# Optimization experiments

Hardware: AMD Instinct MI355X
Metric: run time of the kernel (lower is better)

Reference implementation:

```python
import jax, jax.numpy as jnp
import numpy as np

NUM_ENTS = 100000
NUM_RELS = 237
IN_CH, OUT_CH, KER = 1, 32, 9
IN_DIM = 200
K = 10
OUT_DIM = K * IN_DIM                      # 2000
L_IN = OUT_DIM // IN_CH                   # 2000
L_OUT = (L_IN - KER) // 1 + 1             # 1992
FC_LEN = OUT_CH * L_OUT                   # 63744
BATCH = 512
EPS = 1e-5


def _bn(x, gamma, beta, axes):
    # training-mode batch norm (biased variance), matching torch BatchNorm1d forward
    m = jnp.mean(x, axis=axes, keepdims=True)
    v = jnp.var(x, axis=axes, keepdims=True)
    return (x - m) * jax.lax.rsqrt(v + EPS) * gamma + beta


def setup_inputs() -> dict:
    key = jax.random.key(0)
    ks = jax.random.split(key, 8)
    xavier = lambda k, shape, fan: jax.random.normal(k, shape, jnp.float32) * np.sqrt(2.0 / fan)
    E = xavier(ks[0], (NUM_ENTS, IN_DIM), NUM_ENTS + IN_DIM)
    R = xavier(ks[1], (NUM_RELS * 2, OUT_CH, IN_CH, KER), OUT_CH * IN_CH * KER)
    e_W = xavier(ks[2], (IN_DIM, OUT_DIM), IN_DIM + OUT_DIM)
    fc_W = xavier(ks[3], (IN_DIM, FC_LEN), IN_DIM + FC_LEN)  # torch Linear weight [out, in]
    return {
        "E": E, "R": R, "e_W": e_W, "fc_W": fc_W,
        "bn0_gamma": jnp.ones((IN_DIM,), jnp.float32), "bn0_beta": jnp.zeros((IN_DIM,), jnp.float32),
        "bn1_gamma": jnp.ones((OUT_CH,), jnp.float32), "bn1_beta": jnp.zeros((OUT_CH,), jnp.float32),
        "bn2_gamma": jnp.ones((IN_DIM,), jnp.float32), "bn2_beta": jnp.zeros((IN_DIM,), jnp.float32),
        "e1_idx": jax.random.randint(ks[4], (BATCH,), 0, NUM_ENTS),
        "r_idx": jax.random.randint(ks[5], (BATCH,), 0, NUM_RELS * 2),
    }


def reference(E, R, e_W, fc_W, bn0_gamma, bn0_beta, bn1_gamma, bn1_beta,
              bn2_gamma, bn2_beta, e1_idx, r_idx):
    B = e1_idx.shape[0]
    x = E[e1_idx]                                   # [B, 200]
    x = _bn(x, bn0_gamma, bn0_beta, axes=0)
    x = x @ e_W                                     # [B, 2000]
    k = R[r_idx]                                    # [B, O, C, KER] per-sample filters
    x = x.reshape(B, IN_CH, L_IN)                   # [B, C, L_in]
    # per-sample grouped conv1d == batched small matmul over sliding windows
    win = jnp.arange(L_OUT)[:, None] + jnp.arange(KER)[None, :]  # [L_out, KER]
    patches = x[:, :, win]                          # [B, C, L_out, KER]
    x = jnp.einsum('bock,bclk->bol', k, patches)    # [B, O, L_out]
    x = _bn(x, bn1_gamma[:, None], bn1_beta[:, None], axes=(0, 2))
    x = x.reshape(B, FC_LEN)
    x = x @ fc_W.T                                  # [B, 200]
    x = jnp.tanh(_bn(x, bn2_gamma, bn2_beta, axes=0))
    logits = x @ E.T                                # [B, num_ents]
    return jax.nn.sigmoid(logits)
```

## Files before the change

### kernel.cpp

```cpp
#include <hip/hip_runtime.h>

#define NENT 100000
#define DIM 200
#define ODIM 2000
#define KERN 9
#define OCH 32
#define LOUT 1992
#define FCLEN 63744
#define BSZ 512
#define EPSV 1e-5f
#define KPAD 224
#define NZ 64
#define EROWS 100096

typedef float f32x4 __attribute__((ext_vector_type(4)));
typedef short short8 __attribute__((ext_vector_type(8)));
typedef __bf16 bf16x8 __attribute__((ext_vector_type(8)));
typedef unsigned int uint4v __attribute__((ext_vector_type(4)));
typedef unsigned int uint2v __attribute__((ext_vector_type(2)));

__device__ __forceinline__ unsigned short f2bf(float f) {
  unsigned int u = __float_as_uint(f);
  return (unsigned short)((u + 0x7fffu + ((u >> 16) & 1u)) >> 16);
}

__device__ __forceinline__ float wredf(float v) {
#pragma unroll
  for (int o = 32; o > 0; o >>= 1) v += __shfl_down(v, o, 64);
  return v;
}

__global__ void __launch_bounds__(256) k_probe(float* __restrict__ out) {
  const f32x4 v = (f32x4){0.5f, 0.5f, 0.5f, 0.5f};
  long base = (long)(blockIdx.x % 800) * 16384 + threadIdx.x;
#pragma unroll
  for (int i = 0; i < 64; i++) {
    long idx = base + (long)i * 256;
    if (idx < 12800000L) *(f32x4*)&out[idx * 4] = v;
  }
}

__global__ void __launch_bounds__(256) k_ebf(const float* __restrict__ E,
                                             unsigned short* __restrict__ Ebf) {
  long idx = (long)blockIdx.x * 256 + threadIdx.x;
  int row = (int)(idx / 56), c4 = (int)(idx % 56);
  f32x4 v = (f32x4){0.f, 0.f, 0.f, 0.f};
  if (row < NENT && c4 < 50) v = *(const f32x4*)&E[(long)row * DIM + c4 * 4];
  uint2v pk;
  pk[0] = (unsigned)f2bf(v[0]) | ((unsigned)f2bf(v[1]) << 16);
  pk[1] = (unsigned)f2bf(v[2]) | ((unsigned)f2bf(v[3]) << 16);
  *(uint2v*)&Ebf[(long)row * KPAD + c4 * 4] = pk;
}

__global__ void k_bn0(const float* __restrict__ E, const int* __restrict__ e1,
                      const float* __restrict__ g, const float* __restrict__ b,
                      float* __restrict__ A, float* __restrict__ Bc,
                      float* __restrict__ bias) {
  int f = blockIdx.x, ln = threadIdx.x;
  float s1 = 0.f, s2 = 0.f;
  for (int i = ln; i < BSZ; i += 64) {
    float v = E[(long)e1[i] * DIM + f];
    s1 += v; s2 += v * v;
  }
  s1 = wredf(s1); s2 = wredf(s2);
  if (ln == 0) {
    float m = s1 / BSZ;
    float var = s2 / BSZ - m * m;
    float a = g[f] * rsqrtf(var + EPSV);
    A[f] = a; Bc[f] = b[f] - m * a;
    bias[f] = 0.f;
  }
}

__global__ void __launch_bounds__(256) k_mm1(
    const float* __restrict__ E, const int* __restrict__ e1,
    const float* __restrict__ eW, const float* __restrict__ A,
    const float* __restrict__ Bc, float* __restrict__ x1) {
  __shared__ float xs[16][DIM];
  int t = threadIdx.x;
  int b0 = blockIdx.x * 16, n0 = blockIdx.y * 128;
  for (int idx = t; idx < 16 * DIM; idx += 256) {
    int bi = idx / DIM, f = idx % DIM;
    xs[bi][f] = E[(long)e1[b0 + bi] * DIM + f] * A[f] + Bc[f];
  }
  __syncthreads();
  int lane = t & 63, w = t >> 6;
  int j0 = n0 + lane, j1 = j0 + 64;
  int r0 = w * 4;
  bool c0 = (j0 < ODIM), c1 = (j1 < ODIM);
  float acc[4][2];
#pragma unroll
  for (int r = 0; r < 4; r++) { acc[r][0] = 0.f; acc[r][1] = 0.f; }
  for (int k = 0; k < DIM; k += 4) {
    f32x4 xr[4];
#pragma unroll
    for (int r = 0; r < 4; r++) xr[r] = *(const f32x4*)&xs[r0 + r][k];
#pragma unroll
    for (int kk = 0; kk < 4; kk++) {
      float e0v = c0 ? eW[(long)(k + kk) * ODIM + j0] : 0.f;
      float e1v = c1 ? eW[(long)(k + kk) * ODIM + j1] : 0.f;
#pragma unroll
      for (int r = 0; r < 4; r++) {
        acc[r][0] += xr[r][kk] * e0v;
        acc[r][1] += xr[r][kk] * e1v;
      }
    }
  }
#pragma unroll
  for (int r = 0; r < 4; r++) {
    long base = (long)(b0 + r0 + r) * ODIM;
    if (c0) x1[base + j0] = acc[r][0];
    if (c1) x1[base + j1] = acc[r][1];
  }
}

__global__ void __launch_bounds__(256) k_conv(
    const float* __restrict__ x1, const float* __restrict__ R,
    const int* __restrict__ ridx, unsigned short* __restrict__ convb,
    float* __restrict__ part) {
  __shared__ float xs[ODIM];
  __shared__ float kr[OCH * KERN];
  __shared__ float wr4[4][64];
  int t = threadIdx.x, b = blockIdx.x;
  for (int i = t; i < ODIM; i += 256) xs[i] = x1[(long)b * ODIM + i];
  for (int i = t; i < OCH * KERN; i += 256) kr[i] = R[(long)ridx[b] * (OCH * KERN) + i];
  __syncthreads();
  int l0 = t * 8;
  bool act = (t < 249);
  float w[16];
  if (act) {
#pragma unroll
    for (int i = 0; i < 16; i++) w[i] = xs[l0 + i];
  }
  int wv = t >> 6, ln = t & 63;
  for (int o = 0; o < OCH; o++) {
    float s1 = 0.f, s2 = 0.f;
    if (act) {
      float kk[KERN];
#pragma unroll
      for (int k = 0; k < KERN; k++) kk[k] = kr[o * KERN + k];
      float cb[8];
#pragma unroll
      for (int j = 0; j < 8; j++) {
        float c = 0.f;
#pragma unroll
        for (int k = 0; k < KERN; k++) c += kk[k] * w[j + k];
        cb[j] = c; s1 += c; s2 += c * c;
      }
      uint4v pk;
#pragma unroll
      for (int i = 0; i < 4; i++)
        pk[i] = (unsigned)f2bf(cb[2 * i]) | ((unsigned)f2bf(cb[2 * i + 1]) << 16);
      *(uint4v*)(convb + (long)b * FCLEN + o * LOUT + l0) = pk;
    }
    s1 = wredf(s1); s2 = wredf(s2);
    if (ln == 0) { wr4[wv][o] = s1; wr4[wv][o + 32] = s2; }
  }
  __syncthreads();
  if (t < 64) part[(long)b * 64 + t] = wr4[0][t] + wr4[1][t] + wr4[2][t] + wr4[3][t];
}

__global__ void k_bn1fin(const float* __restrict__ part, const float* __restrict__ g,
                         const float* __restrict__ b, float* __restrict__ a,
                         float* __restrict__ c) {
  __shared__ float sm[4][64];
  __shared__ float tot[64];
  int t = threadIdx.x;
  int si = t >> 6, st = t & 63;
  float s = 0.f;
  for (int i = si; i < BSZ; i += 4) s += part[(long)i * 64 + st];
  sm[si][st] = s;
  __syncthreads();
  if (t < 64) tot[t] = sm[0][t] + sm[1][t] + sm[2][t] + sm[3][t];
  __syncthreads();
  if (t < OCH) {
    float N = (float)BSZ * LOUT;
    float m = tot[t] / N;
    float var = tot[t + 32] / N - m * m;
    float av = g[t] * rsqrtf(var + EPSV);
    a[t] = av; c[t] = b[t] - m * av;
  }
}

__global__ void __launch_bounds__(256) k_fcw(
    const float* __restrict__ fcW, const float* __restrict__ a,
    const float* __restrict__ c, unsigned short* __restrict__ fcWb,
    float* __restrict__ bias) {
  int d = blockIdx.x, o = blockIdx.y, t = threadIdx.x;
  const float* src = fcW + (long)d * FCLEN + o * LOUT;
  unsigned short* dst = fcWb + (long)d * FCLEN + o * LOUT;
  float ao = a[o];
  float s = 0.f;
  if (t < 249) {
    float v[8];
#pragma unroll
    for (int j = 0; j < 8; j++) { v[j] = src[t * 8 + j]; s += v[j]; }
    uint4v pk;
#pragma unroll
    for (int i = 0; i < 4; i++)
      pk[i] = (unsigned)f2bf(v[2 * i] * ao) | ((unsigned)f2bf(v[2 * i + 1] * ao) << 16);
    *(uint4v*)(dst + t * 8) = pk;
  }
  s = wredf(s);
  __shared__ float sm[4];
  if ((t & 63) == 0) sm[t >> 6] = s;
  __syncthreads();
  if (t == 0) atomicAdd(bias + d, c[o] * (sm[0] + sm[1] + sm[2] + sm[3]));
}

__global__ void __launch_bounds__(256) k_gemm_fc(
    const unsigned short* __restrict__ convb, const unsigned short* __restrict__ fcWb,
    float* __restrict__ ypart) {
  __shared__ unsigned short lA[128 * 104];
  __shared__ unsigned short lB[128 * 104];
  int t = threadIdx.x;
  int b0 = blockIdx.x * 128, n0 = blockIdx.y * 128, z = blockIdx.z;
  int s0 = (664 * z) / NZ, s1 = (664 * (z + 1)) / NZ;
  int w = t >> 6, lane = t & 63, lm = lane & 15, quad = lane >> 4;
  int mq = (w >> 1) * 64, nq = (w & 1) * 64;
  f32x4 acc[4][4];
#pragma unroll
  for (int mi = 0; mi < 4; mi++)
#pragma unroll
    for (int ni = 0; ni < 4; ni++) acc[mi][ni] = (f32x4){0.f, 0.f, 0.f, 0.f};
  for (int st = s0; st < s1; st++) {
    long kc = (long)st * 96;
    __syncthreads();
#pragma unroll
    for (int i = 0; i < 6; i++) {
      int cc = t + 256 * i;
      int row = cc / 12, c8 = cc % 12;
      *(uint4v*)&lA[row * 104 + c8 * 8] =
          *(const uint4v*)&convb[(long)(b0 + row) * FCLEN + kc + c8 * 8];
      uint4v bv = (uint4v){0u, 0u, 0u, 0u};
      int nr = n0 + row;
      if (nr < DIM) bv = *(const uint4v*)&fcWb[(long)nr * FCLEN + kc + c8 * 8];
      *(uint4v*)&lB[row * 104 + c8 * 8] = bv;
    }
    __syncthreads();
#pragma unroll
    for (int ks = 0; ks < 96; ks += 32) {
      short8 af[4], bfr[4];
#pragma unroll
      for (int i2 = 0; i2 < 4; i2++) {
        af[i2] = *(const short8*)&lA[(mq + i2 * 16 + lm) * 104 + ks + quad * 8];
        bfr[i2] = *(const short8*)&lB[(nq + i2 * 16 + lm) * 104 + ks + quad * 8];
      }
#pragma unroll
      for (int mi = 0; mi < 4; mi++)
#pragma unroll
        for (int ni = 0; ni < 4; ni++)
          acc[mi][ni] = __builtin_amdgcn_mfma_f32_16x16x32_bf16(
              __builtin_bit_cast(bf16x8, af[mi]), __builtin_bit_cast(bf16x8, bfr[ni]),
              acc[mi][ni], 0, 0, 0);
    }
  }
#pragma unroll
  for (int mi = 0; mi < 4; mi++)
#pragma unroll
    for (int ni = 0; ni < 4; ni++)
#pragma unroll
      for (int r = 0; r < 4; r++) {
        int gm = b0 + mq + mi * 16 + quad * 4 + r;
        int gn = n0 + nq + ni * 16 + lm;
        ypart[((long)z * BSZ + gm) * 256 + gn] = acc[mi][ni][r];
      }
}

__global__ void __launch_bounds__(256) k_yred(
    const float* __restrict__ ypart, const float* __restrict__ bias,
    float* __restrict__ y) {
  int i = blockIdx.x * 256 + threadIdx.x;
  int m = i / DIM, d = i % DIM;
  float s = bias[d];
#pragma unroll 8
  for (int z = 0; z < NZ; z++) s += ypart[((long)z * BSZ + m) * 256 + d];
  y[(long)m * DIM + d] = s;
}

__global__ void k_bn2(const float* __restrict__ y, const float* __restrict__ g,
                      const float* __restrict__ b, unsigned short* __restrict__ xtf) {
  int d = blockIdx.x, ln = threadIdx.x;
  int ks = d >> 5, quad = (d >> 3) & 3, e = d & 7;
  if (d >= DIM) {
    for (int j = 0; j < 8; j++) {
      int row = ln + 64 * j;
      xtf[((((long)(row >> 4) * 7 + ks) * 64) + quad * 16 + (row & 15)) * 8 + e] = 0;
    }
    return;
  }
  float v[8];
  float s1 = 0.f, s2 = 0.f;
#pragma unroll
  for (int j = 0; j < 8; j++) {
    v[j] = y[(long)(ln + 64 * j) * DIM + d];
    s1 += v[j]; s2 += v[j] * v[j];
  }
  s1 = wredf(s1); s2 = wredf(s2);
  s1 = __shfl(s1, 0, 64); s2 = __shfl(s2, 0, 64);
  float m = s1 / BSZ, var = s2 / BSZ - m * m;
  float a = g[d] * rsqrtf(var + EPSV), c = b[d] - m * a;
#pragma unroll
  for (int j = 0; j < 8; j++) {
    int row = ln + 64 * j;
    xtf[((((long)(row >> 4) * 7 + ks) * 64) + quad * 16 + (row & 15)) * 8 + e] =
        f2bf(tanhf(v[j] * a + c));
  }
}

__global__ void __launch_bounds__(512, 4) k_gemmf(
    const unsigned short* __restrict__ xtf, const unsigned short* __restrict__ Ebf,
    float* __restrict__ out) {
  int t = threadIdx.x;
  int w = t >> 6, lane = t & 63, lm = lane & 15, quad = lane >> 4;
  long e0 = (long)blockIdx.x * 64;
  int m0 = w * 64;
  int mtb = w * 4;
  f32x4 acc[4][4];
#pragma unroll
  for (int mi = 0; mi < 4; mi++)
#pragma unroll
    for (int ni = 0; ni < 4; ni++) acc[mi][ni] = (f32x4){0.f, 0.f, 0.f, 0.f};
#pragma unroll
  for (int kk = 0; kk < 7; kk++) {
    short8 bfr[4], af[4];
#pragma unroll
    for (int ni = 0; ni < 4; ni++)
      bfr[ni] = *(const short8*)&Ebf[(e0 + ni * 16 + lm) * KPAD + kk * 32 + quad * 8];
#pragma unroll
    for (int mi = 0; mi < 4; mi++)
      af[mi] = *(const short8*)&xtf[(((long)(mtb + mi) * 7 + kk) * 64 + lane) * 8];
#pragma unroll
    for (int mi = 0; mi < 4; mi++)
#pragma unroll
      for (int ni = 0; ni < 4; ni++)
        acc[mi][ni] = __builtin_amdgcn_mfma_f32_16x16x32_bf16(
            __builtin_bit_cast(bf16x8, af[mi]), __builtin_bit_cast(bf16x8, bfr[ni]),
            acc[mi][ni], 0, 0, 0);
  }
#pragma unroll
  for (int mi = 0; mi < 4; mi++)
#pragma unroll
    for (int ni = 0; ni < 4; ni++) {
      long ge = e0 + ni * 16 + lm;
      bool ok = (ge < NENT);
#pragma unroll
      for (int r = 0; r < 4; r++) {
        int gm = m0 + mi * 16 + quad * 4 + r;
        if (ok) {
          float x = acc[mi][ni][r];
          out[(long)gm * NENT + ge] = 1.f / (1.f + __expf(-x));
        }
      }
    }
}

extern "C" void kernel_launch(void* const* d_in, const int* in_sizes, int n_in,
                              void* d_out, int out_size, void* d_ws, size_t ws_size,
                              hipStream_t stream) {
  const float* E = (const float*)d_in[0];
  const float* R = (const float*)d_in[1];
  const float* eW = (const float*)d_in[2];
  const float* fcW = (const float*)d_in[3];
  const float* bn0g = (const float*)d_in[4];
  const float* bn0b = (const float*)d_in[5];
  const float* bn1g = (const float*)d_in[6];
  const float* bn1b = (const float*)d_in[7];
  const float* bn2g = (const float*)d_in[8];
  const float* bn2b = (const float*)d_in[9];
  const int* e1 = (const int*)d_in[10];
  const int* ridx = (const int*)d_in[11];
  float* outp = (float*)d_out;

  char* p = (char*)d_ws;
  size_t off = 0;
  auto alloc = [&](size_t bytes) -> char* {
    char* r = p + off;
    off = (off + bytes + 255) & ~(size_t)255;
    return r;
  };
  float* x1 = (float*)alloc((size_t)BSZ * ODIM * 4);
  unsigned short* convb = (unsigned short*)alloc((size_t)BSZ * FCLEN * 2);
  unsigned short* fcWb = (unsigned short*)alloc((size_t)DIM * FCLEN * 2);
  unsigned short* Ebf = (unsigned short*)alloc((size_t)EROWS * KPAD * 2);
  float* ypart = (float*)alloc((size_t)NZ * BSZ * 256 * 4);
  float* y = (float*)alloc((size_t)BSZ * DIM * 4);
  unsigned short* xtf = (unsigned short*)alloc((size_t)BSZ * KPAD * 2);
  float* bn0A = (float*)alloc(DIM * 4);
  float* bn0B = (float*)alloc(DIM * 4);
  float* part = (float*)alloc((size_t)BSZ * 64 * 4);
  float* bn1a = (float*)alloc(OCH * 4);
  float* bn1c = (float*)alloc(OCH * 4);
  float* bias = (float*)alloc(DIM * 4);

  k_probe<<<1600, 256, 0, stream>>>(outp);
  k_ebf<<<(EROWS * 56) / 256, 256, 0, stream>>>(E, Ebf);
  k_bn0<<<DIM, 64, 0, stream>>>(E, e1, bn0g, bn0b, bn0A, bn0B, bias);
  k_mm1<<<dim3(32, 16), 256, 0, stream>>>(E, e1, eW, bn0A, bn0B, x1);
  k_conv<<<BSZ, 256, 0, stream>>>(x1, R, ridx, convb, part);
  k_bn1fin<<<1, 256, 0, stream>>>(part, bn1g, bn1b, bn1a, bn1c);
  k_fcw<<<dim3(DIM, OCH), 256, 0, stream>>>(fcW, bn1a, bn1c, fcWb, bias);
  k_gemm_fc<<<dim3(4, 2, NZ), 256, 0, stream>>>(convb, fcWb, ypart);
  k_yred<<<400, 256, 0, stream>>>(ypart, bias, y);
  k_bn2<<<KPAD, 64, 0, stream>>>(y, bn2g, bn2b, xtf);
  k_gemmf<<<1563, 512, 0, stream>>>(xtf, Ebf, outp);
}
```

Measured before the change: 609.6 us.

## Fuse E bf16 conversion into final GEMM and drop probe kernel

Removes the separate kernel that converted the whole 100k-entity embedding table to padded bf16 and instead loads fp32 rows of E directly inside the final logits GEMM, converting to bf16 in registers with K-padding masked to zero. It also deletes a probe kernel that pre-wrote the output buffer. This avoids a full extra read/write pass over E (about 80MB fp32 read plus 45MB bf16 write), at the cost of the GEMM reading twice the bytes per B fragment and doing conversion ALU work in the inner loop.

```diff
diff --git a/kernel.cpp b/kernel.cpp
--- a/kernel.cpp
+++ b/kernel.cpp
@@ -11,7 +11,6 @@
 #define EPSV 1e-5f
 #define KPAD 224
 #define NZ 64
-#define EROWS 100096
 
 typedef float f32x4 __attribute__((ext_vector_type(4)));
 typedef short short8 __attribute__((ext_vector_type(8)));
@@ -28,28 +27,6 @@
 #pragma unroll
   for (int o = 32; o > 0; o >>= 1) v += __shfl_down(v, o, 64);
   return v;
-}
-
-__global__ void __launch_bounds__(256) k_probe(float* __restrict__ out) {
-  const f32x4 v = (f32x4){0.5f, 0.5f, 0.5f, 0.5f};
-  long base = (long)(blockIdx.x % 800) * 16384 + threadIdx.x;
-#pragma unroll
-  for (int i = 0; i < 64; i++) {
-    long idx = base + (long)i * 256;
-    if (idx < 12800000L) *(f32x4*)&out[idx * 4] = v;
-  }
-}
-
-__global__ void __launch_bounds__(256) k_ebf(const float* __restrict__ E,
-                                             unsigned short* __restrict__ Ebf) {
-  long idx = (long)blockIdx.x * 256 + threadIdx.x;
-  int row = (int)(idx / 56), c4 = (int)(idx % 56);
-  f32x4 v = (f32x4){0.f, 0.f, 0.f, 0.f};
-  if (row < NENT && c4 < 50) v = *(const f32x4*)&E[(long)row * DIM + c4 * 4];
-  uint2v pk;
-  pk[0] = (unsigned)f2bf(v[0]) | ((unsigned)f2bf(v[1]) << 16);
-  pk[1] = (unsigned)f2bf(v[2]) | ((unsigned)f2bf(v[3]) << 16);
-  *(uint2v*)&Ebf[(long)row * KPAD + c4 * 4] = pk;
 }
 
 __global__ void k_bn0(const float* __restrict__ E, const int* __restrict__ e1,
@@ -309,24 +286,42 @@
 }
 
 __global__ void __launch_bounds__(512, 4) k_gemmf(
-    const unsigned short* __restrict__ xtf, const unsigned short* __restrict__ Ebf,
+    const unsigned short* __restrict__ xtf, const float* __restrict__ E,
     float* __restrict__ out) {
   int t = threadIdx.x;
   int w = t >> 6, lane = t & 63, lm = lane & 15, quad = lane >> 4;
   long e0 = (long)blockIdx.x * 64;
   int m0 = w * 64;
   int mtb = w * 4;
+  int brow[4];
+#pragma unroll
+  for (int ni = 0; ni < 4; ni++) {
+    long ge = e0 + ni * 16 + lm;
+    brow[ni] = (int)((ge < NENT ? ge : (long)(NENT - 1)) * DIM);
+  }
   f32x4 acc[4][4];
 #pragma unroll
   for (int mi = 0; mi < 4; mi++)
 #pragma unroll
     for (int ni = 0; ni < 4; ni++) acc[mi][ni] = (f32x4){0.f, 0.f, 0.f, 0.f};
+  const short8 z8 = {0, 0, 0, 0, 0, 0, 0, 0};
 #pragma unroll
   for (int kk = 0; kk < 7; kk++) {
+    int k0 = kk * 32 + quad * 8;
+    bool kval = (k0 <= DIM - 8);
+    int kc = kval ? k0 : 0;
     short8 bfr[4], af[4];
 #pragma unroll
-    for (int ni = 0; ni < 4; ni++)
-      bfr[ni] = *(const short8*)&Ebf[(e0 + ni * 16 + lm) * KPAD + kk * 32 + quad * 8];
+    for (int ni = 0; ni < 4; ni++) {
+      f32x4 lo = *(const f32x4*)&E[(long)brow[ni] + kc];
+      f32x4 hi = *(const f32x4*)&E[(long)brow[ni] + kc + 4];
+      short8 pk;
+      pk[0] = (short)f2bf(lo[0]); pk[1] = (short)f2bf(lo[1]);
+      pk[2] = (short)f2bf(lo[2]); pk[3] = (short)f2bf(lo[3]);
+      pk[4] = (short)f2bf(hi[0]); pk[5] = (short)f2bf(hi[1]);
+      pk[6] = (short)f2bf(hi[2]); pk[7] = (short)f2bf(hi[3]);
+      bfr[ni] = kval ? pk : z8;
+    }
 #pragma unroll
     for (int mi = 0; mi < 4; mi++)
       af[mi] = *(const short8*)&xtf[(((long)(mtb + mi) * 7 + kk) * 64 + lane) * 8];
@@ -382,7 +377,6 @@
   float* x1 = (float*)alloc((size_t)BSZ * ODIM * 4);
   unsigned short* convb = (unsigned short*)alloc((size_t)BSZ * FCLEN * 2);
   unsigned short* fcWb = (unsigned short*)alloc((size_t)DIM * FCLEN * 2);
-  unsigned short* Ebf = (unsigned short*)alloc((size_t)EROWS * KPAD * 2);
   float* ypart = (float*)alloc((size_t)NZ * BSZ * 256 * 4);
   float* y = (float*)alloc((size_t)BSZ * DIM * 4);
   unsigned short* xtf = (unsigned short*)alloc((size_t)BSZ * KPAD * 2);
@@ -393,8 +387,6 @@
   float* bn1c = (float*)alloc(OCH * 4);
   float* bias = (float*)alloc(DIM * 4);
 
-  k_probe<<<1600, 256, 0, stream>>>(outp);
-  k_ebf<<<(EROWS * 56) / 256, 256, 0, stream>>>(E, Ebf);
   k_bn0<<<DIM, 64, 0, stream>>>(E, e1, bn0g, bn0b, bn0A, bn0B, bias);
   k_mm1<<<dim3(32, 16), 256, 0, stream>>>(E, e1, eW, bn0A, bn0B, x1);
   k_conv<<<BSZ, 256, 0, stream>>>(x1, R, ridx, convb, part);
@@ -403,5 +395,5 @@
   k_gemm_fc<<<dim3(4, 2, NZ), 256, 0, stream>>>(convb, fcWb, ypart);
   k_yred<<<400, 256, 0, stream>>>(ypart, bias, y);
   k_bn2<<<KPAD, 64, 0, stream>>>(y, bn2g, bn2b, xtf);
-  k_gemmf<<<1563, 512, 0, stream>>>(xtf, Ebf, outp);
-}
+  k_gemmf<<<1563, 512, 0, stream>>>(xtf, E, outp);
+}
```

Measured after the change: 572.7 us. 1.06x faster.
